# Kernel tuning notes

Measured on AMD Instinct MI355X. Metric: run time of the kernel, lower is better.

## Reference

```python
import jax, jax.numpy as jnp
import numpy as np

B, T1, D, K = 8, 513, 768, 8192  # batch, tokens incl. CLS, feature dim, codebook size


def setup_inputs() -> dict:
    key = jax.random.key(0)
    k1, k2 = jax.random.split(key)
    representation = jax.random.normal(k1, (B, T1, D), dtype=jnp.float32)
    centroids = jax.random.normal(k2, (K, D), dtype=jnp.float32)
    return {"representation": representation, "centroids": centroids}


def reference(representation, centroids):
    # quant_mem_efficient: drop first (CLS) token, L2-distance argmin over codebook
    rep = representation[:, 1:, :]                        # [B, T, D]
    norm_rep = jnp.sum(rep * rep, axis=-1, keepdims=True)  # [B, T, 1]
    norm_cent = jnp.sum(centroids * centroids, axis=-1)    # [K]
    dot = jnp.einsum('btd,kd->btk', rep, centroids)        # [B, T, K]
    distances = norm_rep + norm_cent[None, None, :] - 2.0 * dot
    tokens = jnp.argmin(distances, axis=-1)                # [B, T] int
    # unquant: embedding gather
    quantized = jnp.take(centroids, tokens, axis=0)        # [B, T, D]
    return tokens, quantized
```

## Files before the change

### kernel.cpp

```cpp
#include <hip/hip_runtime.h>
#include <stdint.h>

#define BT 4096
#define KC 8192
#define DD 768
#define T_STRIDE 513
#define DELTA 20.0f

typedef int   v4i  __attribute__((ext_vector_type(4)));
typedef float f32x4 __attribute__((ext_vector_type(4)));

#define GLD16(gp, lp)                                                       \
  __builtin_amdgcn_global_load_lds(                                         \
      (__attribute__((address_space(1))) void*)(gp),                        \
      (__attribute__((address_space(3))) void*)(lp), 16, 0, 0)

__device__ __forceinline__ unsigned int sortable_bits(float d) {
  unsigned int bits = __float_as_uint(d);
  return (bits & 0x80000000u) ? ~bits : (bits | 0x80000000u);
}

__global__ __launch_bounds__(256) void quant_kernel(
    const float* __restrict__ rep, const float* __restrict__ cent,
    int8_t* __restrict__ a8, int8_t* __restrict__ b8,
    float* __restrict__ s_a, float* __restrict__ s_b,
    float* __restrict__ norm_cent) {
  int wid  = (blockIdx.x * blockDim.x + threadIdx.x) >> 6;
  int lane = threadIdx.x & 63;
  const float4* s4;
  int8_t* dst;
  float* sdst;
  float* ndst = nullptr;
  if (wid < BT) {
    int b = wid >> 9, tt = wid & 511;
    s4 = (const float4*)(rep + (size_t)(b * T_STRIDE + 1 + tt) * DD);
    dst = a8 + (size_t)wid * DD;
    sdst = s_a + wid;
  } else {
    int k = wid - BT;
    if (k >= KC) return;
    s4 = (const float4*)(cent + (size_t)k * DD);
    dst = b8 + (size_t)k * DD;
    sdst = s_b + k;
    ndst = norm_cent + k;
  }
  float4 v[3];
  float m = 0.f, nrm = 0.f;
  #pragma unroll
  for (int i = 0; i < 3; ++i) {
    v[i] = s4[lane + i * 64];
    m = fmaxf(m, fmaxf(fmaxf(fabsf(v[i].x), fabsf(v[i].y)),
                       fmaxf(fabsf(v[i].z), fabsf(v[i].w))));
    nrm += v[i].x * v[i].x + v[i].y * v[i].y + v[i].z * v[i].z + v[i].w * v[i].w;
  }
  #pragma unroll
  for (int off = 32; off; off >>= 1) m = fmaxf(m, __shfl_xor(m, off, 64));
  const float rs = (m > 0.f) ? 127.0f / m : 0.f;
  unsigned* d32 = (unsigned*)dst;
  #pragma unroll
  for (int i = 0; i < 3; ++i) {
    int q0 = (int)rintf(v[i].x * rs);
    int q1 = (int)rintf(v[i].y * rs);
    int q2 = (int)rintf(v[i].z * rs);
    int q3 = (int)rintf(v[i].w * rs);
    unsigned pk = (unsigned)(q0 & 255) | ((unsigned)(q1 & 255) << 8) |
                  ((unsigned)(q2 & 255) << 16) | ((unsigned)(q3 & 255) << 24);
    d32[lane + i * 64] = pk;
  }
  if (ndst) {
    #pragma unroll
    for (int off = 32; off; off >>= 1) nrm += __shfl_down(nrm, off, 64);
  }
  if (lane == 0) {
    *sdst = m / 127.0f;
    if (ndst) *ndst = nrm;
  }
}

__global__ __launch_bounds__(256, 2) void mfma_i8_cand(
    const int8_t* __restrict__ a8,
    const int8_t* __restrict__ b8,
    const float* __restrict__ s_a, const float* __restrict__ s_b,
    const float* __restrict__ norm_cent,
    float* __restrict__ LMin, unsigned long long* __restrict__ Mask) {
  __shared__ __attribute__((aligned(16))) int8_t As[128 * 128];
  __shared__ __attribute__((aligned(16))) int8_t Bs[128 * 128];

  const int tid = threadIdx.x;
  const int w = tid >> 6, l = tid & 63;
  const int bm0 = blockIdx.x * 128;
  const int bn0 = blockIdx.y * 128;

  const int srow   = l >> 3;
  const int schunk = (l & 7) ^ srow;
  size_t goffA[4], goffB[4];
  int8_t *ldsA[4], *ldsB[4];
  #pragma unroll
  for (int j2 = 0; j2 < 4; ++j2) {
    const int j = w * 4 + j2;
    goffA[j2] = (size_t)(bm0 + j * 8 + srow) * DD + schunk * 16;
    goffB[j2] = (size_t)(bn0 + j * 8 + srow) * DD + schunk * 16;
    ldsA[j2] = As + j * 8 * 128;
    ldsB[j2] = Bs + j * 8 * 128;
  }

  const int wm = (w & 1) * 64;
  const int wn = (w >> 1) * 64;
  const int sub = l & 15, q = l >> 4;

  v4i acc[4][4] = {};

  for (int kin = 0; kin < DD; kin += 128) {
    __syncthreads();
    #pragma unroll
    for (int j2 = 0; j2 < 4; ++j2) {
      GLD16(b8 + goffA[j2] + kin, ldsA[j2]);
      GLD16(a8 + goffB[j2] + kin, ldsB[j2]);
    }
    __syncthreads();

    #pragma unroll
    for (int kk = 0; kk < 2; ++kk) {
      v4i af[4], bf[4];
      #pragma unroll
      for (int i = 0; i < 4; ++i) {
        const int arow = wm + i * 16 + sub;
        const int brow = wn + i * 16 + sub;
        const int c = q + kk * 4;
        af[i] = *(const v4i*)(As + arow * 128 + ((c ^ (arow & 7)) * 16));
        bf[i] = *(const v4i*)(Bs + brow * 128 + ((c ^ (brow & 7)) * 16));
      }
      #pragma unroll
      for (int mt = 0; mt < 4; ++mt)
        #pragma unroll
        for (int nt = 0; nt < 4; ++nt)
          asm volatile("v_mfma_i32_16x16x64_i8 %0, %1, %2, %0"
                       : "+v"(acc[mt][nt])
                       : "v"(af[mt]), "v"(bf[nt]));
    }
  }
  asm volatile("s_nop 7\n\ts_nop 7\n\ts_nop 7" ::: "memory");

  const int g = (bm0 >> 6) + (w & 1);
  float ncv[4][4], sbv[4][4];
  #pragma unroll
  for (int mt = 0; mt < 4; ++mt)
    #pragma unroll
    for (int r = 0; r < 4; ++r) {
      const int k = bm0 + wm + mt * 16 + q * 4 + r;
      ncv[mt][r] = norm_cent[k];
      sbv[mt][r] = s_b[k];
    }

  #pragma unroll
  for (int nt = 0; nt < 4; ++nt) {
    const int t = bn0 + wn + nt * 16 + sub;
    const float sa2 = 2.0f * s_a[t];
    float d[4][4];
    float dmin = 3.4e38f;
    #pragma unroll
    for (int mt = 0; mt < 4; ++mt)
      #pragma unroll
      for (int r = 0; r < 4; ++r) {
        d[mt][r] = ncv[mt][r] - sa2 * sbv[mt][r] * (float)acc[mt][nt][r];
        dmin = fminf(dmin, d[mt][r]);
      }
    dmin = fminf(dmin, __shfl_xor(dmin, 16, 64));
    dmin = fminf(dmin, __shfl_xor(dmin, 32, 64));
    const float thresh = dmin + DELTA;
    unsigned long long pm = 0;
    #pragma unroll
    for (int mt = 0; mt < 4; ++mt)
      #pragma unroll
      for (int r = 0; r < 4; ++r)
        if (d[mt][r] <= thresh) pm |= 1ull << (mt * 16 + q * 4 + r);
    pm |= (unsigned long long)__shfl_xor((long long)pm, 16, 64);
    pm |= (unsigned long long)__shfl_xor((long long)pm, 32, 64);
    if (q == 0) {
      LMin[(size_t)t * 128 + g] = dmin;
      Mask[(size_t)t * 128 + g] = pm;
    }
  }
}

__global__ __launch_bounds__(256) void refine_kernel(
    const float* __restrict__ LMin, const unsigned long long* __restrict__ Mask,
    const float* __restrict__ rep, const float* __restrict__ cent,
    const float* __restrict__ norm_cent,
    float* __restrict__ out_tokens, float* __restrict__ out_q) {
  const int w = threadIdx.x >> 6, l = threadIdx.x & 63;
  const int t = blockIdx.x * 4 + w;
  if (t >= BT) return;

  const float lm0 = LMin[(size_t)t * 128 + l];
  const float lm1 = LMin[(size_t)t * 128 + 64 + l];
  float v = fminf(lm0, lm1);
  #pragma unroll
  for (int off = 32; off; off >>= 1) v = fminf(v, __shfl_xor(v, off, 64));
  const float thresh = v + DELTA;
  unsigned long long gm0 = __ballot(lm0 <= thresh);
  unsigned long long gm1 = __ballot(lm1 <= thresh);

  const int b_ = t >> 9, tt = t & 511;
  const float* rrow = rep + (size_t)(b_ * T_STRIDE + 1 + tt) * DD;
  unsigned long long bestE = ~0ull;

  #pragma unroll
  for (int half = 0; half < 2; ++half) {
    unsigned long long gmask = half ? gm1 : gm0;
    while (gmask) {
      const int h = __ffsll((unsigned long long)gmask) - 1;
      gmask &= gmask - 1;
      unsigned long long mask = Mask[(size_t)t * 128 + half * 64 + h];
      while (mask) {
        const int bit = __ffsll((unsigned long long)mask) - 1;
        mask &= mask - 1;
        const int k = (half * 64 + h) * 64 + bit;
        const float* crow = cent + (size_t)k * DD;
        float part = 0.f;
        #pragma unroll
        for (int j = 0; j < 12; ++j)
          part += rrow[l + j * 64] * crow[l + j * 64];
        #pragma unroll
        for (int off = 32; off; off >>= 1) part += __shfl_down(part, off, 64);
        if (l == 0) {
          float d = norm_cent[k] - 2.0f * part;
          unsigned long long p =
              ((unsigned long long)sortable_bits(d) << 32) | (unsigned)k;
          if (p < bestE) bestE = p;
        }
      }
    }
  }
  int kb0 = (l == 0) ? (int)(bestE & 0xFFFFFFFFull) : 0;
  const int kbest = __shfl(kb0, 0, 64);
  if (l == 0) out_tokens[t] = (float)kbest;
  const float4* src = (const float4*)(cent + (size_t)kbest * DD);
  float4* dst = (float4*)(out_q + (size_t)t * DD);
  #pragma unroll
  for (int j = 0; j < 3; ++j) dst[l + j * 64] = src[l + j * 64];
}

#define FBM 64
#define FBN 64
#define FBK 16
#define FNSPLIT 16
__global__ __launch_bounds__(256) void norms_only_kernel(
    const float* __restrict__ rep, const float* __restrict__ cent,
    float* __restrict__ norm_rep, float* __restrict__ norm_cent) {
  int wid  = (blockIdx.x * blockDim.x + threadIdx.x) >> 6;
  int lane = threadIdx.x & 63;
  const float* src;
  float* nd;
  if (wid < BT) {
    int b = wid >> 9, tt = wid & 511;
    src = rep + (size_t)(b * T_STRIDE + 1 + tt) * DD;
    nd = norm_rep + wid;
  } else {
    int k = wid - BT;
    if (k >= KC) return;
    src = cent + (size_t)k * DD;
    nd = norm_cent + k;
  }
  float s = 0.f;
  for (int j = lane; j < DD; j += 64) { float v = src[j]; s += v * v; }
  #pragma unroll
  for (int off = 32; off; off >>= 1) s += __shfl_down(s, off, 64);
  if (lane == 0) *nd = s;
}

__global__ __launch_bounds__(256) void fp32_argmin_gemm(
    const float* __restrict__ rep, const float* __restrict__ cent,
    const float* __restrict__ norm_rep, const float* __restrict__ norm_cent,
    unsigned long long* __restrict__ packed) {
  __shared__ float Asf[FBK][FBM];
  __shared__ float Bsf[FBK][FBN];
  const int tid = threadIdx.x;
  const int m0  = blockIdx.x * FBM;
  const int kbase = blockIdx.y * (KC / FNSPLIT);
  const int tx = tid & 15, ty = tid >> 4;
  const int ldr = tid >> 2, ldc = (tid & 3) * 4;
  const int t_ld = m0 + ldr;
  const float* arow =
      rep + (size_t)((t_ld >> 9) * T_STRIDE + 1 + (t_ld & 511)) * DD + ldc;
  unsigned long long best[4];
  #pragma unroll
  for (int i = 0; i < 4; ++i) best[i] = ~0ull;
  float nr[4];
  #pragma unroll
  for (int i = 0; i < 4; ++i) nr[i] = norm_rep[m0 + ty * 4 + i];
  for (int nt = 0; nt < (KC / FNSPLIT) / FBN; ++nt) {
    const int n0 = kbase + nt * FBN;
    const float* brow = cent + (size_t)(n0 + ldr) * DD + ldc;
    float acc[4][4];
    #pragma unroll
    for (int i = 0; i < 4; ++i)
      #pragma unroll
      for (int j = 0; j < 4; ++j) acc[i][j] = 0.f;
    for (int d0 = 0; d0 < DD; d0 += FBK) {
      float4 av = *(const float4*)(arow + d0);
      float4 bv = *(const float4*)(brow + d0);
      __syncthreads();
      Asf[ldc + 0][ldr] = av.x; Asf[ldc + 1][ldr] = av.y;
      Asf[ldc + 2][ldr] = av.z; Asf[ldc + 3][ldr] = av.w;
      Bsf[ldc + 0][ldr] = bv.x; Bsf[ldc + 1][ldr] = bv.y;
      Bsf[ldc + 2][ldr] = bv.z; Bsf[ldc + 3][ldr] = bv.w;
      __syncthreads();
      #pragma unroll
      for (int kk = 0; kk < FBK; ++kk) {
        float4 a4 = *(const float4*)&Asf[kk][ty * 4];
        float4 b4 = *(const float4*)&Bsf[kk][tx * 4];
        float a[4] = {a4.x, a4.y, a4.z, a4.w};
        float b[4] = {b4.x, b4.y, b4.z, b4.w};
        #pragma unroll
        for (int i = 0; i < 4; ++i)
          #pragma unroll
          for (int j = 0; j < 4; ++j) acc[i][j] += a[i] * b[j];
      }
    }
    #pragma unroll
    for (int i = 0; i < 4; ++i) {
      #pragma unroll
      for (int j = 0; j < 4; ++j) {
        int k = n0 + tx * 4 + j;
        float d = (nr[i] + norm_cent[k]) - 2.0f * acc[i][j];
        unsigned long long p =
            ((unsigned long long)sortable_bits(d) << 32) | (unsigned int)k;
        if (p < best[i]) best[i] = p;
      }
    }
  }
  #pragma unroll
  for (int off = 1; off < 16; off <<= 1) {
    #pragma unroll
    for (int i = 0; i < 4; ++i) {
      unsigned long long o =
          (unsigned long long)__shfl_xor((long long)best[i], off, 64);
      if (o < best[i]) best[i] = o;
    }
  }
  if (tx == 0) {
    #pragma unroll
    for (int i = 0; i < 4; ++i)
      atomicMin(&packed[m0 + ty * 4 + i], best[i]);
  }
}

__global__ __launch_bounds__(192) void gather_kernel(
    const unsigned long long* __restrict__ packed,
    const float* __restrict__ cent,
    float* __restrict__ out_tokens, float* __restrict__ out_q) {
  int t = blockIdx.x;
  unsigned int k = (unsigned int)(packed[t] & 0xFFFFFFFFull);
  if (threadIdx.x == 0) out_tokens[t] = (float)k;
  const float4* src = (const float4*)(cent + (size_t)k * DD);
  float4* dst = (float4*)(out_q + (size_t)t * DD);
  dst[threadIdx.x] = src[threadIdx.x];
}

extern "C" void kernel_launch(void* const* d_in, const int* in_sizes, int n_in,
                              void* d_out, int out_size, void* d_ws, size_t ws_size,
                              hipStream_t stream) {
  const float* rep  = (const float*)d_in[0];
  const float* cent = (const float*)d_in[1];
  float* out = (float*)d_out;

  const size_t SZ_A8 = (size_t)BT * DD;
  const size_t SZ_B8 = (size_t)KC * DD;
  const size_t SZ_LM = (size_t)BT * 128 * 4;
  const size_t SZ_MK = (size_t)BT * 128 * 8;
  const size_t OFF_SA = SZ_A8 + SZ_B8 + SZ_LM + SZ_MK;
  const size_t OFF_SB = OFF_SA + 16384;
  const size_t OFF_NC = OFF_SB + 32768;
  const size_t WS_A   = OFF_NC + 32768;

  if (ws_size >= WS_A) {
    int8_t* a8 = (int8_t*)d_ws;
    int8_t* b8 = (int8_t*)((char*)d_ws + SZ_A8);
    float* LMin = (float*)((char*)d_ws + SZ_A8 + SZ_B8);
    unsigned long long* Mask =
        (unsigned long long*)((char*)d_ws + SZ_A8 + SZ_B8 + SZ_LM);
    float* s_a = (float*)((char*)d_ws + OFF_SA);
    float* s_b = (float*)((char*)d_ws + OFF_SB);
    float* norm_cent = (float*)((char*)d_ws + OFF_NC);

    quant_kernel<<<3072, 256, 0, stream>>>(rep, cent, a8, b8, s_a, s_b,
                                           norm_cent);
    dim3 grid(KC / 128, BT / 128);
    mfma_i8_cand<<<grid, 256, 0, stream>>>(a8, b8, s_a, s_b, norm_cent,
                                           LMin, Mask);
    refine_kernel<<<BT / 4, 256, 0, stream>>>(LMin, Mask, rep, cent,
                                              norm_cent, out, out + BT);
  } else {
    unsigned long long* packed = (unsigned long long*)d_ws;
    float* norm_rep  = (float*)((char*)d_ws + 32768);
    float* norm_cent = (float*)((char*)d_ws + 49152);

    hipMemsetAsync(packed, 0xFF, BT * sizeof(unsigned long long), stream);
    norms_only_kernel<<<3072, 256, 0, stream>>>(rep, cent, norm_rep, norm_cent);
    dim3 grid(BT / FBM, FNSPLIT);
    fp32_argmin_gemm<<<grid, 256, 0, stream>>>(rep, cent, norm_rep, norm_cent,
                                               packed);
    gather_kernel<<<BT, 192, 0, stream>>>(packed, cent, out, out + BT);
  }
}
```

Measured before the change: 135.6 us.

## Double-buffer LDS tiles in int8 MFMA candidate kernel to overlap loads with compute

```diff
diff --git a/kernel.cpp b/kernel.cpp
--- a/kernel.cpp
+++ b/kernel.cpp
@@ -83,8 +83,8 @@
     const float* __restrict__ s_a, const float* __restrict__ s_b,
     const float* __restrict__ norm_cent,
     float* __restrict__ LMin, unsigned long long* __restrict__ Mask) {
-  __shared__ __attribute__((aligned(16))) int8_t As[128 * 128];
-  __shared__ __attribute__((aligned(16))) int8_t Bs[128 * 128];
+  __shared__ __attribute__((aligned(16))) int8_t As[2][128 * 128];
+  __shared__ __attribute__((aligned(16))) int8_t Bs[2][128 * 128];
 
   const int tid = threadIdx.x;
   const int w = tid >> 6, l = tid & 63;
@@ -94,14 +94,13 @@
   const int srow   = l >> 3;
   const int schunk = (l & 7) ^ srow;
   size_t goffA[4], goffB[4];
-  int8_t *ldsA[4], *ldsB[4];
+  int soff[4];
   #pragma unroll
   for (int j2 = 0; j2 < 4; ++j2) {
     const int j = w * 4 + j2;
     goffA[j2] = (size_t)(bm0 + j * 8 + srow) * DD + schunk * 16;
     goffB[j2] = (size_t)(bn0 + j * 8 + srow) * DD + schunk * 16;
-    ldsA[j2] = As + j * 8 * 128;
-    ldsB[j2] = Bs + j * 8 * 128;
+    soff[j2] = j * 8 * 128;
   }
 
   const int wm = (w & 1) * 64;
@@ -110,15 +109,14 @@
 
   v4i acc[4][4] = {};
 
-  for (int kin = 0; kin < DD; kin += 128) {
-    __syncthreads();
+  auto STAGE = [&](int buf, int kin) {
     #pragma unroll
     for (int j2 = 0; j2 < 4; ++j2) {
-      GLD16(b8 + goffA[j2] + kin, ldsA[j2]);
-      GLD16(a8 + goffB[j2] + kin, ldsB[j2]);
-    }
-    __syncthreads();
-
+      GLD16(b8 + goffA[j2] + kin, As[buf] + soff[j2]);
+      GLD16(a8 + goffB[j2] + kin, Bs[buf] + soff[j2]);
+    }
+  };
+  auto COMPUTE = [&](int buf) {
     #pragma unroll
     for (int kk = 0; kk < 2; ++kk) {
       v4i af[4], bf[4];
@@ -127,8 +125,8 @@
         const int arow = wm + i * 16 + sub;
         const int brow = wn + i * 16 + sub;
         const int c = q + kk * 4;
-        af[i] = *(const v4i*)(As + arow * 128 + ((c ^ (arow & 7)) * 16));
-        bf[i] = *(const v4i*)(Bs + brow * 128 + ((c ^ (brow & 7)) * 16));
+        af[i] = *(const v4i*)(As[buf] + arow * 128 + ((c ^ (arow & 7)) * 16));
+        bf[i] = *(const v4i*)(Bs[buf] + brow * 128 + ((c ^ (brow & 7)) * 16));
       }
       #pragma unroll
       for (int mt = 0; mt < 4; ++mt)
@@ -138,7 +136,19 @@
                        : "+v"(acc[mt][nt])
                        : "v"(af[mt]), "v"(bf[nt]));
     }
-  }
+  };
+
+  STAGE(0, 0);
+  __syncthreads();
+
+  #pragma unroll
+  for (int t = 0; t < 6; ++t) {
+    const int cur = t & 1;
+    if (t < 5) STAGE(cur ^ 1, (t + 1) * 128);
+    COMPUTE(cur);
+    if (t < 5) __syncthreads();
+  }
+
   asm volatile("s_nop 7\n\ts_nop 7\n\ts_nop 7" ::: "memory");
 
   const int g = (bm0 >> 6) + (w & 1);
```

Result: slower. 145.3 us (+7.2%).

## Enlarge int8 MFMA candidate tiles to 256x256 with double-buffered LDS pipelining

Applied to the files above, without the earlier changes.

```diff
diff --git a/kernel.cpp b/kernel.cpp
--- a/kernel.cpp
+++ b/kernel.cpp
@@ -77,110 +77,159 @@
   }
 }
 
-__global__ __launch_bounds__(256, 2) void mfma_i8_cand(
+__global__ __launch_bounds__(512, 2) void mfma_i8_cand(
     const int8_t* __restrict__ a8,
     const int8_t* __restrict__ b8,
     const float* __restrict__ s_a, const float* __restrict__ s_b,
     const float* __restrict__ norm_cent,
     float* __restrict__ LMin, unsigned long long* __restrict__ Mask) {
-  __shared__ __attribute__((aligned(16))) int8_t As[128 * 128];
-  __shared__ __attribute__((aligned(16))) int8_t Bs[128 * 128];
+  __shared__ __attribute__((aligned(16))) int8_t As[2][256 * 128];
+  __shared__ __attribute__((aligned(16))) int8_t Bs[2][256 * 128];
 
   const int tid = threadIdx.x;
   const int w = tid >> 6, l = tid & 63;
-  const int bm0 = blockIdx.x * 128;
-  const int bn0 = blockIdx.y * 128;
+
+  const int lb  = blockIdx.x + blockIdx.y * 32;
+  const int tgt = (lb & 7) * 64 + (lb >> 3);
+  const int bm0 = (tgt >> 4) * 256;
+  const int bn0 = (tgt & 15) * 256;
 
   const int srow   = l >> 3;
   const int schunk = (l & 7) ^ srow;
-  size_t goffA[4], goffB[4];
-  int8_t *ldsA[4], *ldsB[4];
-  #pragma unroll
-  for (int j2 = 0; j2 < 4; ++j2) {
-    const int j = w * 4 + j2;
-    goffA[j2] = (size_t)(bm0 + j * 8 + srow) * DD + schunk * 16;
-    goffB[j2] = (size_t)(bn0 + j * 8 + srow) * DD + schunk * 16;
-    ldsA[j2] = As + j * 8 * 128;
-    ldsB[j2] = Bs + j * 8 * 128;
-  }
-
-  const int wm = (w & 1) * 64;
-  const int wn = (w >> 1) * 64;
+  const size_t gA0 = (size_t)(bm0 + w * 32 + srow) * DD + schunk * 16;
+  const size_t gB0 = (size_t)(bn0 + w * 32 + srow) * DD + schunk * 16;
+  const int ls0 = w * 4096;
+
+  const int wm = (w >> 2) * 128;
+  const int wn = (w & 3) * 64;
   const int sub = l & 15, q = l >> 4;
 
-  v4i acc[4][4] = {};
-
-  for (int kin = 0; kin < DD; kin += 128) {
-    __syncthreads();
-    #pragma unroll
-    for (int j2 = 0; j2 < 4; ++j2) {
-      GLD16(b8 + goffA[j2] + kin, ldsA[j2]);
-      GLD16(a8 + goffB[j2] + kin, ldsB[j2]);
-    }
-    __syncthreads();
-
-    #pragma unroll
-    for (int kk = 0; kk < 2; ++kk) {
-      v4i af[4], bf[4];
-      #pragma unroll
-      for (int i = 0; i < 4; ++i) {
-        const int arow = wm + i * 16 + sub;
-        const int brow = wn + i * 16 + sub;
-        const int c = q + kk * 4;
-        af[i] = *(const v4i*)(As + arow * 128 + ((c ^ (arow & 7)) * 16));
-        bf[i] = *(const v4i*)(Bs + brow * 128 + ((c ^ (brow & 7)) * 16));
+  v4i acc[8][4] = {};
+
+#define STAGE(j, buf, kin)                                                   \
+  do {                                                                       \
+    GLD16(b8 + gA0 + (j) * 8 * DD + (kin), As[buf] + ls0 + (j) * 1024);      \
+    GLD16(a8 + gB0 + (j) * 8 * DD + (kin), Bs[buf] + ls0 + (j) * 1024);      \
+  } while (0)
+
+#define LDA(dst, buf, mh, kk)                                                \
+  do {                                                                       \
+    _Pragma("unroll") for (int i_ = 0; i_ < 4; ++i_) {                       \
+      const int row_ = wm + ((mh) * 4 + i_) * 16 + sub;                      \
+      dst[i_] = *(const v4i*)(As[buf] + row_ * 128 +                         \
+                              (((q + (kk) * 4) ^ (row_ & 7)) * 16));         \
+    }                                                                        \
+  } while (0)
+
+#define LDB(dst, buf, kk)                                                    \
+  do {                                                                       \
+    _Pragma("unroll") for (int i_ = 0; i_ < 4; ++i_) {                       \
+      const int row_ = wn + i_ * 16 + sub;                                   \
+      dst[i_] = *(const v4i*)(Bs[buf] + row_ * 128 +                         \
+                              (((q + (kk) * 4) ^ (row_ & 7)) * 16));         \
+    }                                                                        \
+  } while (0)
+
+#define MM(mh, af, bf)                                                       \
+  do {                                                                       \
+    __builtin_amdgcn_s_setprio(1);                                           \
+    _Pragma("unroll") for (int mt_ = 0; mt_ < 4; ++mt_)                      \
+        _Pragma("unroll") for (int nt_ = 0; nt_ < 4; ++nt_)                  \
+            asm volatile("v_mfma_i32_16x16x64_i8 %0, %1, %2, %0"             \
+                         : "+v"(acc[(mh) * 4 + mt_][nt_])                    \
+                         : "v"(af[mt_]), "v"(bf[nt_]));                      \
+    __builtin_amdgcn_s_setprio(0);                                           \
+  } while (0)
+
+#define PHASE_SYNC()                                                         \
+  do {                                                                       \
+    __builtin_amdgcn_s_barrier();                                            \
+    asm volatile("s_waitcnt lgkmcnt(0)" ::: "memory");                       \
+    __builtin_amdgcn_sched_barrier(0);                                       \
+  } while (0)
+
+  #pragma unroll
+  for (int j = 0; j < 4; ++j) STAGE(j, 0, 0);
+  __syncthreads();
+
+  #pragma unroll
+  for (int kt = 0; kt < 6; ++kt) {
+    const int cur = kt & 1, nxt = cur ^ 1;
+    const int kin = (kt + 1) * 128;
+    v4i fa[4], fb[4], fb2[4];
+    LDA(fa, cur, 0, 0);
+    LDB(fb, cur, 0);
+    if (kt < 5) { STAGE(0, nxt, kin); STAGE(1, nxt, kin); }
+    PHASE_SYNC();
+    MM(0, fa, fb);
+    __builtin_amdgcn_s_barrier();
+    LDA(fa, cur, 1, 0);
+    if (kt < 5) { STAGE(2, nxt, kin); STAGE(3, nxt, kin); }
+    PHASE_SYNC();
+    MM(1, fa, fb);
+    __builtin_amdgcn_s_barrier();
+    LDA(fa, cur, 0, 1);
+    LDB(fb2, cur, 1);
+    PHASE_SYNC();
+    MM(0, fa, fb2);
+    __builtin_amdgcn_s_barrier();
+    LDA(fa, cur, 1, 1);
+    PHASE_SYNC();
+    MM(1, fa, fb2);
+    if (kt < 5) asm volatile("s_waitcnt vmcnt(0)" ::: "memory");
+    __builtin_amdgcn_s_barrier();
+    __builtin_amdgcn_sched_barrier(0);
+  }
+
+  asm volatile("s_nop 7\n\ts_nop 7\n\ts_nop 7" ::: "memory");
+
+  #pragma unroll
+  for (int half = 0; half < 2; ++half) {
+    const int g = ((bm0 + wm) >> 6) + half;
+    float nc[4][4], sb2[4][4];
+    #pragma unroll
+    for (int mt = 0; mt < 4; ++mt)
+      #pragma unroll
+      for (int r = 0; r < 4; ++r) {
+        const int k = bm0 + wm + (half * 4 + mt) * 16 + q * 4 + r;
+        nc[mt][r] = norm_cent[k];
+        sb2[mt][r] = 2.0f * s_b[k];
       }
+    #pragma unroll
+    for (int nt = 0; nt < 4; ++nt) {
+      const int t = bn0 + wn + nt * 16 + sub;
+      const float sa = s_a[t];
+      float d[4][4];
+      float dmin = 3.4e38f;
       #pragma unroll
       for (int mt = 0; mt < 4; ++mt)
         #pragma unroll
-        for (int nt = 0; nt < 4; ++nt)
-          asm volatile("v_mfma_i32_16x16x64_i8 %0, %1, %2, %0"
-                       : "+v"(acc[mt][nt])
-                       : "v"(af[mt]), "v"(bf[nt]));
+        for (int r = 0; r < 4; ++r) {
+          d[mt][r] = nc[mt][r] - sa * sb2[mt][r] * (float)acc[half * 4 + mt][nt][r];
+          dmin = fminf(dmin, d[mt][r]);
+        }
+      dmin = fminf(dmin, __shfl_xor(dmin, 16, 64));
+      dmin = fminf(dmin, __shfl_xor(dmin, 32, 64));
+      const float thresh = dmin + DELTA;
+      unsigned long long pm = 0;
+      #pragma unroll
+      for (int mt = 0; mt < 4; ++mt)
+        #pragma unroll
+        for (int r = 0; r < 4; ++r)
+          if (d[mt][r] <= thresh) pm |= 1ull << (mt * 16 + q * 4 + r);
+      pm |= (unsigned long long)__shfl_xor((long long)pm, 16, 64);
+      pm |= (unsigned long long)__shfl_xor((long long)pm, 32, 64);
+      if (q == 0) {
+        LMin[(size_t)t * 128 + g] = dmin;
+        Mask[(size_t)t * 128 + g] = pm;
+      }
     }
   }
-  asm volatile("s_nop 7\n\ts_nop 7\n\ts_nop 7" ::: "memory");
-
-  const int g = (bm0 >> 6) + (w & 1);
-  float ncv[4][4], sbv[4][4];
-  #pragma unroll
-  for (int mt = 0; mt < 4; ++mt)
-    #pragma unroll
-    for (int r = 0; r < 4; ++r) {
-      const int k = bm0 + wm + mt * 16 + q * 4 + r;
-      ncv[mt][r] = norm_cent[k];
-      sbv[mt][r] = s_b[k];
-    }
-
-  #pragma unroll
-  for (int nt = 0; nt < 4; ++nt) {
-    const int t = bn0 + wn + nt * 16 + sub;
-    const float sa2 = 2.0f * s_a[t];
-    float d[4][4];
-    float dmin = 3.4e38f;
-    #pragma unroll
-    for (int mt = 0; mt < 4; ++mt)
-      #pragma unroll
-      for (int r = 0; r < 4; ++r) {
-        d[mt][r] = ncv[mt][r] - sa2 * sbv[mt][r] * (float)acc[mt][nt][r];
-        dmin = fminf(dmin, d[mt][r]);
-      }
-    dmin = fminf(dmin, __shfl_xor(dmin, 16, 64));
-    dmin = fminf(dmin, __shfl_xor(dmin, 32, 64));
-    const float thresh = dmin + DELTA;
-    unsigned long long pm = 0;
-    #pragma unroll
-    for (int mt = 0; mt < 4; ++mt)
-      #pragma unroll
-      for (int r = 0; r < 4; ++r)
-        if (d[mt][r] <= thresh) pm |= 1ull << (mt * 16 + q * 4 + r);
-    pm |= (unsigned long long)__shfl_xor((long long)pm, 16, 64);
-    pm |= (unsigned long long)__shfl_xor((long long)pm, 32, 64);
-    if (q == 0) {
-      LMin[(size_t)t * 128 + g] = dmin;
-      Mask[(size_t)t * 128 + g] = pm;
-    }
-  }
+#undef STAGE
+#undef LDA
+#undef LDB
+#undef MM
+#undef PHASE_SYNC
 }
 
 __global__ __launch_bounds__(256) void refine_kernel(
@@ -386,8 +435,8 @@
 
     quant_kernel<<<3072, 256, 0, stream>>>(rep, cent, a8, b8, s_a, s_b,
                                            norm_cent);
-    dim3 grid(KC / 128, BT / 128);
-    mfma_i8_cand<<<grid, 256, 0, stream>>>(a8, b8, s_a, s_b, norm_cent,
+    dim3 grid(KC / 256, BT / 256);
+    mfma_i8_cand<<<grid, 512, 0, stream>>>(a8, b8, s_a, s_b, norm_cent,
                                            LMin, Mask);
     refine_kernel<<<BT / 4, 256, 0, stream>>>(LMin, Mask, rep, cent,
                                               norm_cent, out, out + BT);
```

New measurement: 141.1 us. 4.1% more time.

## Triple-buffer int8 MFMA K-loop with async LDS loads and occupancy 3

Applied to the files above, without the earlier changes.

```diff
diff --git a/kernel.cpp b/kernel.cpp
--- a/kernel.cpp
+++ b/kernel.cpp
@@ -77,68 +77,69 @@
   }
 }
 
-__global__ __launch_bounds__(256, 2) void mfma_i8_cand(
+__global__ __launch_bounds__(256, 3) void mfma_i8_cand(
     const int8_t* __restrict__ a8,
     const int8_t* __restrict__ b8,
     const float* __restrict__ s_a, const float* __restrict__ s_b,
     const float* __restrict__ norm_cent,
     float* __restrict__ LMin, unsigned long long* __restrict__ Mask) {
-  __shared__ __attribute__((aligned(16))) int8_t As[128 * 128];
-  __shared__ __attribute__((aligned(16))) int8_t Bs[128 * 128];
+  __shared__ __attribute__((aligned(16))) int8_t As[3][128 * 64];
+  __shared__ __attribute__((aligned(16))) int8_t Bs[3][128 * 64];
 
   const int tid = threadIdx.x;
   const int w = tid >> 6, l = tid & 63;
   const int bm0 = blockIdx.x * 128;
   const int bn0 = blockIdx.y * 128;
 
-  const int srow   = l >> 3;
-  const int schunk = (l & 7) ^ srow;
-  size_t goffA[4], goffB[4];
-  int8_t *ldsA[4], *ldsB[4];
-  #pragma unroll
-  for (int j2 = 0; j2 < 4; ++j2) {
-    const int j = w * 4 + j2;
-    goffA[j2] = (size_t)(bm0 + j * 8 + srow) * DD + schunk * 16;
-    goffB[j2] = (size_t)(bn0 + j * 8 + srow) * DD + schunk * 16;
-    ldsA[j2] = As + j * 8 * 128;
-    ldsB[j2] = Bs + j * 8 * 128;
-  }
+  const int srow   = tid >> 2;
+  const int schunk = (tid & 3) ^ ((tid >> 3) & 3);
+  const size_t gA0 = (size_t)(bm0 + srow) * DD + schunk * 16;
+  const size_t gB0 = (size_t)(bn0 + srow) * DD + schunk * 16;
+  const int ldst = tid * 16;
 
   const int wm = (w & 1) * 64;
   const int wn = (w >> 1) * 64;
   const int sub = l & 15, q = l >> 4;
+  const int rslot = (q ^ ((sub >> 1) & 3)) * 16;
 
   v4i acc[4][4] = {};
 
-  for (int kin = 0; kin < DD; kin += 128) {
-    __syncthreads();
-    #pragma unroll
-    for (int j2 = 0; j2 < 4; ++j2) {
-      GLD16(b8 + goffA[j2] + kin, ldsA[j2]);
-      GLD16(a8 + goffB[j2] + kin, ldsB[j2]);
-    }
-    __syncthreads();
-
-    #pragma unroll
-    for (int kk = 0; kk < 2; ++kk) {
-      v4i af[4], bf[4];
-      #pragma unroll
-      for (int i = 0; i < 4; ++i) {
-        const int arow = wm + i * 16 + sub;
-        const int brow = wn + i * 16 + sub;
-        const int c = q + kk * 4;
-        af[i] = *(const v4i*)(As + arow * 128 + ((c ^ (arow & 7)) * 16));
-        bf[i] = *(const v4i*)(Bs + brow * 128 + ((c ^ (brow & 7)) * 16));
-      }
-      #pragma unroll
-      for (int mt = 0; mt < 4; ++mt)
-        #pragma unroll
-        for (int nt = 0; nt < 4; ++nt)
-          asm volatile("v_mfma_i32_16x16x64_i8 %0, %1, %2, %0"
-                       : "+v"(acc[mt][nt])
-                       : "v"(af[mt]), "v"(bf[nt]));
-    }
-  }
+#define STAGE(s)                                                             \
+  do {                                                                       \
+    const int b_ = (s) % 3;                                                  \
+    GLD16(b8 + gA0 + (s) * 64,           As[b_] + ldst);                     \
+    GLD16(b8 + gA0 + 64 * DD + (s) * 64, As[b_] + 4096 + ldst);              \
+    GLD16(a8 + gB0 + (s) * 64,           Bs[b_] + ldst);                     \
+    GLD16(a8 + gB0 + 64 * DD + (s) * 64, Bs[b_] + 4096 + ldst);              \
+  } while (0)
+
+  STAGE(0);
+  STAGE(1);
+
+  #pragma unroll
+  for (int s = 0; s < 12; ++s) {
+    if (s < 11) asm volatile("s_waitcnt vmcnt(4)" ::: "memory");
+    else        asm volatile("s_waitcnt vmcnt(0)" ::: "memory");
+    __builtin_amdgcn_s_barrier();
+    __builtin_amdgcn_sched_barrier(0);
+    const int buf = s % 3;
+    v4i af[4], bf[4];
+    #pragma unroll
+    for (int i = 0; i < 4; ++i) {
+      af[i] = *(const v4i*)(As[buf] + (wm + i * 16 + sub) * 64 + rslot);
+      bf[i] = *(const v4i*)(Bs[buf] + (wn + i * 16 + sub) * 64 + rslot);
+    }
+    if (s < 10) STAGE(s + 2);
+    #pragma unroll
+    for (int mt = 0; mt < 4; ++mt)
+      #pragma unroll
+      for (int nt = 0; nt < 4; ++nt)
+        asm volatile("v_mfma_i32_16x16x64_i8 %0, %1, %2, %0"
+                     : "+v"(acc[mt][nt])
+                     : "v"(af[mt]), "v"(bf[nt]));
+  }
+#undef STAGE
+
   asm volatile("s_nop 7\n\ts_nop 7\n\ts_nop 7" ::: "memory");
 
   const int g = (bm0 >> 6) + (w & 1);
```

Result: slower. 144.9 us (+6.9%).
